# Kernel optimization log

Hardware: AMD Instinct MI355X
Metric: run time of the kernel (lower is better)

Reference implementation:

```python
import jax, jax.numpy as jnp
import numpy as np

N_EMBD = 512
HEAD_SIZE = 64
B, T = 256, 256


def setup_inputs() -> dict:
    key = jax.random.key(0)
    ks = jax.random.split(key, 7)
    s = 1.0 / np.sqrt(N_EMBD)
    return {
        "x": jax.random.normal(ks[0], (B, T, N_EMBD), dtype=jnp.float32),
        "Wk": jax.random.uniform(ks[1], (N_EMBD, HEAD_SIZE), jnp.float32, -s, s),
        "bk": jax.random.uniform(ks[2], (HEAD_SIZE,), jnp.float32, -s, s),
        "Wq": jax.random.uniform(ks[3], (N_EMBD, HEAD_SIZE), jnp.float32, -s, s),
        "bq": jax.random.uniform(ks[4], (HEAD_SIZE,), jnp.float32, -s, s),
        "Wv": jax.random.uniform(ks[5], (N_EMBD, HEAD_SIZE), jnp.float32, -s, s),
        "bv": jax.random.uniform(ks[6], (HEAD_SIZE,), jnp.float32, -s, s),
    }


def reference(x, Wk, bk, Wq, bq, Wv, bv):
    # Single-head causal self-attention (dropout = identity in eval mode).
    Bq, Tq, C = x.shape
    k = x @ Wk + bk        # [B, T, H]
    q = x @ Wq + bq        # [B, T, H]
    v = x @ Wv + bv        # [B, T, H]
    scale = 1.0 / jnp.sqrt(jnp.asarray(k.shape[-1], x.dtype))
    scores = jnp.einsum('bth,bsh->bts', q, k) * scale  # [B, T, T]
    causal = jnp.tril(jnp.ones((Tq, Tq), dtype=bool))
    scores = jnp.where(causal, scores, -jnp.inf)
    attn = jax.nn.softmax(scores, axis=-1)
    return jnp.einsum('bts,bsh->bth', attn, v)  # [B, T, H]
```

## Files before the change

kernel.cpp:

```cpp
#include <hip/hip_runtime.h>
#include <stdint.h>

typedef __attribute__((ext_vector_type(8))) short bf16x8;
typedef __attribute__((ext_vector_type(4))) float f32x4;

#if __has_builtin(__builtin_amdgcn_exp2f)
#define EXP2F(x) __builtin_amdgcn_exp2f(x)
#else
#define EXP2F(x) exp2f(x)
#endif

__device__ __forceinline__ short f2bf(float f) {
    union { float f; uint32_t u; } c; c.f = f;
    return (short)((c.u + 0x7fffu + ((c.u >> 16) & 1u)) >> 16);
}

typedef __attribute__((address_space(1))) void gvoid;
typedef __attribute__((address_space(3))) void lvoid;
__device__ __forceinline__ void async_cp16(const void* g, void* l) {
    __builtin_amdgcn_global_load_lds((gvoid*)g, (lvoid*)l, 16, 0, 0);
}

__global__ void prep_kernel(const float* __restrict__ Wk, const float* __restrict__ bk,
                            const float* __restrict__ Wq, const float* __restrict__ bq,
                            const float* __restrict__ Wv, const float* __restrict__ bv,
                            short* __restrict__ Wt2g, float* __restrict__ bcat) {
    const int col = blockIdx.x;
    const float* W; const float* bb; int c0;
    if (col < 64)       { W = Wk; bb = bk; c0 = col; }
    else if (col < 128) { W = Wq; bb = bq; c0 = col - 64; }
    else                { W = Wv; bb = bv; c0 = col - 128; }
    for (int c = threadIdx.x; c < 512; c += blockDim.x)
        Wt2g[(c >> 5) * (192 * 32) + col * 32 + (c & 31)] = f2bf(W[(size_t)c * 64 + c0]);
    if (threadIdx.x == 0) bcat[col] = bb[c0];
}

#define PSTR 40

__global__ __launch_bounds__(1024, 4) void fused_kernel(
    const float* __restrict__ x, const short* __restrict__ Wt2g,
    const float* __restrict__ bcat, float* __restrict__ out) {
    extern __shared__ __align__(16) char smem[];

    const int tid = threadIdx.x;
    const int wave = tid >> 6, lane = tid & 63;
    const int quad = lane >> 4, l16 = lane & 15;
    const int b = blockIdx.x;

    const int rg = wave >> 2, cg = wave & 3;

    f32x4 acc[4][3];
#pragma unroll
    for (int m = 0; m < 4; m++)
#pragma unroll
        for (int j = 0; j < 3; j++) acc[m][j] = (f32x4){0.f, 0.f, 0.f, 0.f};

    const float* xg = x + ((size_t)b * 256 + wave * 16 + l16) * 512 + quad * 8;

#define STAGE_W(kc, bufp)                                                           \
    if (wave < 12) {                                                                \
        async_cp16(Wt2g + (size_t)(kc) * 6144 + wave * 512 + lane * 8,              \
                   smem + 32768 + (bufp) * 12288 + wave * 1024);                    \
    }

    STAGE_W(0, 0)
    f32x4 xr0 = *(const f32x4*)xg;
    f32x4 xr1 = *(const f32x4*)(xg + 4);
    {
        bf16x8 v;
#pragma unroll
        for (int i = 0; i < 4; i++) { v[i] = f2bf(xr0[i]); v[4 + i] = f2bf(xr1[i]); }
        *(bf16x8*)((short*)smem + wave * 512 + lane * 8) = v;
    }
    __syncthreads();

    for (int kc = 0; kc < 16; kc++) {
        const int buf = kc & 1;
        if (kc < 15) {
            STAGE_W(kc + 1, buf ^ 1)
            xr0 = *(const f32x4*)(xg + (kc + 1) * 32);
            xr1 = *(const f32x4*)(xg + (kc + 1) * 32 + 4);
        }
        const short* wb = (const short*)(smem + 32768 + buf * 12288);
        bf16x8 bfr0 = *(const bf16x8*)&wb[(cg * 48 + l16) * 32 + quad * 8];
        bf16x8 bfr1 = *(const bf16x8*)&wb[(cg * 48 + 16 + l16) * 32 + quad * 8];
        bf16x8 bfr2 = *(const bf16x8*)&wb[(cg * 48 + 32 + l16) * 32 + quad * 8];
        const short* xbr = (const short*)smem + buf * 8192;
#pragma unroll
        for (int m = 0; m < 4; m++) {
            bf16x8 afr = *(const bf16x8*)&xbr[(rg * 4 + m) * 512 + lane * 8];
            acc[m][0] = __builtin_amdgcn_mfma_f32_16x16x32_bf16(afr, bfr0, acc[m][0], 0, 0, 0);
            acc[m][1] = __builtin_amdgcn_mfma_f32_16x16x32_bf16(afr, bfr1, acc[m][1], 0, 0, 0);
            acc[m][2] = __builtin_amdgcn_mfma_f32_16x16x32_bf16(afr, bfr2, acc[m][2], 0, 0, 0);
        }
        if (kc < 15) {
            bf16x8 v;
#pragma unroll
            for (int i = 0; i < 4; i++) { v[i] = f2bf(xr0[i]); v[4 + i] = f2bf(xr1[i]); }
            *(bf16x8*)((short*)smem + (buf ^ 1) * 8192 + wave * 512 + lane * 8) = v;
        }
        __syncthreads();
    }

    short* Ks  = (short*)smem;
    short* Qs  = (short*)(smem + 32768);
    short* Vts = (short*)(smem + 65536);
    short* Ps  = (short*)(smem + 98304);
#pragma unroll
    for (int j = 0; j < 3; j++) {
        const int col = cg * 48 + j * 16 + l16;
        const float bias = bcat[col];
        const int h = col & 63;
        const int sel = col >> 6;
#pragma unroll
        for (int m = 0; m < 4; m++) {
#pragma unroll
            for (int r = 0; r < 4; r++) {
                const short v = f2bf(acc[m][j][r] + bias);
                const int row = rg * 64 + m * 16 + quad * 4 + r;
                if (sel == 0)
                    Ks[row * 64 + (((h >> 3) ^ (row & 7)) << 3) + (h & 7)] = v;
                else if (sel == 1)
                    Qs[row * 64 + (((h >> 3) ^ (row & 7)) << 3) + (h & 7)] = v;
                else
                    Vts[h * 256 + (((row >> 3) ^ (h & 7)) << 3) + (row & 7)] = v;
            }
        }
    }
    __syncthreads();

    const int qt = ((wave >> 2) << 2) | ((wave & 3) ^ (wave >> 2));
    const float sc2 = 0.125f * 1.44269504088896340736f;
    short* myP = Ps + wave * (16 * PSTR);

    const int qrow = qt * 16 + l16;
    const int sw = l16 & 7;
    bf16x8 qf0 = *(const bf16x8*)&Qs[qrow * 64 + ((quad ^ sw) << 3)];
    bf16x8 qf1 = *(const bf16x8*)&Qs[qrow * 64 + (((4 + quad) ^ sw) << 3)];

    f32x4 St[16];
#pragma unroll
    for (int i = 0; i < 16; i++) St[i] = (f32x4){0.f, 0.f, 0.f, 0.f};
#pragma unroll
    for (int nt = 0; nt < 16; nt++) if (nt <= qt) {
        const int krow = nt * 16 + l16;
        bf16x8 kf0 = *(const bf16x8*)&Ks[krow * 64 + ((quad ^ sw) << 3)];
        bf16x8 kf1 = *(const bf16x8*)&Ks[krow * 64 + (((4 + quad) ^ sw) << 3)];
        St[nt] = __builtin_amdgcn_mfma_f32_16x16x32_bf16(qf0, kf0, St[nt], 0, 0, 0);
        St[nt] = __builtin_amdgcn_mfma_f32_16x16x32_bf16(qf1, kf1, St[nt], 0, 0, 0);
    }

    const int rowq = qt * 16 + quad * 4;
    float mx[4], ls[4];
#pragma unroll
    for (int r = 0; r < 4; r++) mx[r] = -3.0e38f;
#pragma unroll
    for (int nt = 0; nt < 16; nt++) if (nt <= qt) {
        const int cs = nt * 16 + l16;
#pragma unroll
        for (int r = 0; r < 4; r++) {
            float s = (cs <= rowq + r) ? St[nt][r] * sc2 : -3.0e38f;
            St[nt][r] = s;
            mx[r] = fmaxf(mx[r], s);
        }
    }
#pragma unroll
    for (int d = 1; d < 16; d <<= 1)
#pragma unroll
        for (int r = 0; r < 4; r++)
            mx[r] = fmaxf(mx[r], __shfl_xor(mx[r], d, 64));
#pragma unroll
    for (int r = 0; r < 4; r++) ls[r] = 0.f;
#pragma unroll
    for (int nt = 0; nt < 16; nt++) if (nt <= qt) {
#pragma unroll
        for (int r = 0; r < 4; r++) {
            float p = EXP2F(St[nt][r] - mx[r]);
            St[nt][r] = p;
            ls[r] += p;
        }
    }
#pragma unroll
    for (int d = 1; d < 16; d <<= 1)
#pragma unroll
        for (int r = 0; r < 4; r++)
            ls[r] += __shfl_xor(ls[r], d, 64);

    f32x4 O[4];
#pragma unroll
    for (int i = 0; i < 4; i++) O[i] = (f32x4){0.f, 0.f, 0.f, 0.f};
    const int nch = (qt + 2) >> 1;
#pragma unroll
    for (int c2 = 0; c2 < 8; c2++) if (c2 < nch) {
#pragma unroll
        for (int t2i = 0; t2i < 2; t2i++) {
            const int nt = c2 * 2 + t2i;
#pragma unroll
            for (int r = 0; r < 4; r++)
                myP[(quad * 4 + r) * PSTR + t2i * 16 + l16] = f2bf(St[nt][r]);
        }
        bf16x8 pf = *(const bf16x8*)&myP[l16 * PSTR + quad * 8];
#pragma unroll
        for (int ht = 0; ht < 4; ht++) {
            const int h = ht * 16 + l16;
            bf16x8 vf = *(const bf16x8*)&Vts[h * 256 + (((c2 * 4 + quad) ^ (h & 7)) << 3)];
            O[ht] = __builtin_amdgcn_mfma_f32_16x16x32_bf16(pf, vf, O[ht], 0, 0, 0);
        }
    }

    float rls[4];
#pragma unroll
    for (int r = 0; r < 4; r++) rls[r] = 1.0f / ls[r];
#pragma unroll
    for (int ht = 0; ht < 4; ht++)
#pragma unroll
        for (int r = 0; r < 4; r++)
            out[((size_t)b * 256 + rowq + r) * 64 + ht * 16 + l16] = O[ht][r] * rls[r];
#undef STAGE_W
}

extern "C" void kernel_launch(void* const* d_in, const int* in_sizes, int n_in,
                              void* d_out, int out_size, void* d_ws, size_t ws_size,
                              hipStream_t stream) {
    const float* x  = (const float*)d_in[0];
    const float* Wk = (const float*)d_in[1];
    const float* bk = (const float*)d_in[2];
    const float* Wq = (const float*)d_in[3];
    const float* bq = (const float*)d_in[4];
    const float* Wv = (const float*)d_in[5];
    const float* bv = (const float*)d_in[6];
    float* out = (float*)d_out;

    char* ws = (char*)d_ws;
    short* Wt2g = (short*)(ws);
    float* bcat = (float*)(ws + 196608);

    const int smem_bytes = 118784;
    (void)hipFuncSetAttribute((const void*)fused_kernel,
                              hipFuncAttributeMaxDynamicSharedMemorySize, smem_bytes);

    prep_kernel<<<192, 256, 0, stream>>>(Wk, bk, Wq, bq, Wv, bv, Wt2g, bcat);
    fused_kernel<<<256, 1024, smem_bytes, stream>>>(x, Wt2g, bcat, out);
}
```

Baseline: 222.0 us.

## Stream x as fp32 via async LDS copies in a triple-buffered projection pipeline

The QKV projection loop now loads x as raw fp32 straight into LDS with global_load_lds, and the W tiles come the same way. It uses three stages with explicit vmcnt waits and raw barriers in place of the register-staged double buffer. Conversion to bf16 moves to the LDS-read side, and both the x and W tiles use XOR swizzles to avoid bank conflicts. The aim is to keep more loads in flight and take the global load latency off the critical path. The cost is more LDS (135 KB), which limits residency to one block per CU, plus hand-tuned wait counts that are fragile.

```diff
diff --git a/kernel.cpp b/kernel.cpp
--- a/kernel.cpp
+++ b/kernel.cpp
@@ -30,8 +30,11 @@
     if (col < 64)       { W = Wk; bb = bk; c0 = col; }
     else if (col < 128) { W = Wq; bb = bq; c0 = col - 64; }
     else                { W = Wv; bb = bv; c0 = col - 128; }
-    for (int c = threadIdx.x; c < 512; c += blockDim.x)
-        Wt2g[(c >> 5) * (192 * 32) + col * 32 + (c & 31)] = f2bf(W[(size_t)c * 64 + c0]);
+    for (int c = threadIdx.x; c < 512; c += blockDim.x) {
+        const int k5 = c & 31;
+        Wt2g[(c >> 5) * 6144 + col * 32 + ((((k5 >> 3) ^ (col & 3)) << 3)) + (k5 & 7)] =
+            f2bf(W[(size_t)c * 64 + c0]);
+    }
     if (threadIdx.x == 0) bcat[col] = bb[c0];
 }
 
@@ -46,7 +49,6 @@
     const int wave = tid >> 6, lane = tid & 63;
     const int quad = lane >> 4, l16 = lane & 15;
     const int b = blockIdx.x;
-
     const int rg = wave >> 2, cg = wave & 3;
 
     f32x4 acc[4][3];
@@ -55,52 +57,70 @@
 #pragma unroll
         for (int j = 0; j < 3; j++) acc[m][j] = (f32x4){0.f, 0.f, 0.f, 0.f};
 
-    const float* xg = x + ((size_t)b * 256 + wave * 16 + l16) * 512 + quad * 8;
-
-#define STAGE_W(kc, bufp)                                                           \
-    if (wave < 12) {                                                                \
-        async_cp16(Wt2g + (size_t)(kc) * 6144 + wave * 512 + lane * 8,              \
-                   smem + 32768 + (bufp) * 12288 + wave * 1024);                    \
-    }
-
-    STAGE_W(0, 0)
-    f32x4 xr0 = *(const f32x4*)xg;
-    f32x4 xr1 = *(const f32x4*)(xg + 4);
-    {
-        bf16x8 v;
-#pragma unroll
-        for (int i = 0; i < 4; i++) { v[i] = f2bf(xr0[i]); v[4 + i] = f2bf(xr1[i]); }
-        *(bf16x8*)((short*)smem + wave * 512 + lane * 8) = v;
-    }
+    const float* xsrc = x + (size_t)b * 256 * 512;
+    const int xr = lane >> 3, xsl = lane & 7;
+    const int bsw = (quad ^ (l16 & 3)) << 3;
+    const int xq0 = ((2 * quad) ^ (l16 & 7)) << 2;
+    const int xq1 = ((2 * quad + 1) ^ (l16 & 7)) << 2;
+
+#define XS(d) (smem + (d) * 32768)
+#define WSB(d) (smem + 98304 + (d) * 12288)
+#define STAGE(kc, d)                                                                     \
+    {                                                                                    \
+        async_cp16(xsrc + (size_t)(wave * 8 + xr) * 512 + (kc) * 32 + ((xsl ^ xr) << 2), \
+                   XS(d) + wave * 1024);                                                 \
+        async_cp16(xsrc + (size_t)((wave + 16) * 8 + xr) * 512 + (kc) * 32 +             \
+                       ((xsl ^ xr) << 2),                                                \
+                   XS(d) + (wave + 16) * 1024);                                          \
+        if (wave < 12)                                                                   \
+            async_cp16(Wt2g + (size_t)(kc) * 6144 + wave * 512 + lane * 8,               \
+                       WSB(d) + wave * 1024);                                            \
+    }
+#define FENCE() asm volatile("" ::: "memory")
+
+    auto COMPUTE = [&](int d) {
+        const short* wb = (const short*)WSB(d);
+        bf16x8 bf0 = *(const bf16x8*)&wb[(cg * 48 + l16) * 32 + bsw];
+        bf16x8 bf1 = *(const bf16x8*)&wb[(cg * 48 + 16 + l16) * 32 + bsw];
+        bf16x8 bf2 = *(const bf16x8*)&wb[(cg * 48 + 32 + l16) * 32 + bsw];
+        const float* xb = (const float*)XS(d);
+        const int rbase = (rg * 64 + l16) * 32;
+#pragma unroll
+        for (int m = 0; m < 4; m++) {
+            f32x4 u0 = *(const f32x4*)&xb[rbase + m * 512 + xq0];
+            f32x4 u1 = *(const f32x4*)&xb[rbase + m * 512 + xq1];
+            bf16x8 a;
+#pragma unroll
+            for (int i = 0; i < 4; i++) { a[i] = f2bf(u0[i]); a[4 + i] = f2bf(u1[i]); }
+            acc[m][0] = __builtin_amdgcn_mfma_f32_16x16x32_bf16(a, bf0, acc[m][0], 0, 0, 0);
+            acc[m][1] = __builtin_amdgcn_mfma_f32_16x16x32_bf16(a, bf1, acc[m][1], 0, 0, 0);
+            acc[m][2] = __builtin_amdgcn_mfma_f32_16x16x32_bf16(a, bf2, acc[m][2], 0, 0, 0);
+        }
+    };
+
+    STAGE(0, 0) STAGE(1, 1) STAGE(2, 2)
+
+    for (int kc = 0; kc < 14; ++kc) {
+        const int d = kc % 3;
+        if (wave < 12) asm volatile("s_waitcnt vmcnt(6)" ::: "memory");
+        else           asm volatile("s_waitcnt vmcnt(4)" ::: "memory");
+        __builtin_amdgcn_s_barrier();
+        FENCE();
+        COMPUTE(d);
+        __builtin_amdgcn_s_barrier();
+        FENCE();
+        if (kc < 13) STAGE(kc + 3, d)
+    }
+    if (wave < 12) asm volatile("s_waitcnt vmcnt(3)" ::: "memory");
+    else           asm volatile("s_waitcnt vmcnt(2)" ::: "memory");
+    __builtin_amdgcn_s_barrier();
+    FENCE();
+    COMPUTE(2);
+    asm volatile("s_waitcnt vmcnt(0)" ::: "memory");
+    __builtin_amdgcn_s_barrier();
+    FENCE();
+    COMPUTE(0);
     __syncthreads();
-
-    for (int kc = 0; kc < 16; kc++) {
-        const int buf = kc & 1;
-        if (kc < 15) {
-            STAGE_W(kc + 1, buf ^ 1)
-            xr0 = *(const f32x4*)(xg + (kc + 1) * 32);
-            xr1 = *(const f32x4*)(xg + (kc + 1) * 32 + 4);
-        }
-        const short* wb = (const short*)(smem + 32768 + buf * 12288);
-        bf16x8 bfr0 = *(const bf16x8*)&wb[(cg * 48 + l16) * 32 + quad * 8];
-        bf16x8 bfr1 = *(const bf16x8*)&wb[(cg * 48 + 16 + l16) * 32 + quad * 8];
-        bf16x8 bfr2 = *(const bf16x8*)&wb[(cg * 48 + 32 + l16) * 32 + quad * 8];
-        const short* xbr = (const short*)smem + buf * 8192;
-#pragma unroll
-        for (int m = 0; m < 4; m++) {
-            bf16x8 afr = *(const bf16x8*)&xbr[(rg * 4 + m) * 512 + lane * 8];
-            acc[m][0] = __builtin_amdgcn_mfma_f32_16x16x32_bf16(afr, bfr0, acc[m][0], 0, 0, 0);
-            acc[m][1] = __builtin_amdgcn_mfma_f32_16x16x32_bf16(afr, bfr1, acc[m][1], 0, 0, 0);
-            acc[m][2] = __builtin_amdgcn_mfma_f32_16x16x32_bf16(afr, bfr2, acc[m][2], 0, 0, 0);
-        }
-        if (kc < 15) {
-            bf16x8 v;
-#pragma unroll
-            for (int i = 0; i < 4; i++) { v[i] = f2bf(xr0[i]); v[4 + i] = f2bf(xr1[i]); }
-            *(bf16x8*)((short*)smem + (buf ^ 1) * 8192 + wave * 512 + lane * 8) = v;
-        }
-        __syncthreads();
-    }
 
     short* Ks  = (short*)smem;
     short* Qs  = (short*)(smem + 32768);
@@ -216,7 +236,10 @@
 #pragma unroll
         for (int r = 0; r < 4; r++)
             out[((size_t)b * 256 + rowq + r) * 64 + ht * 16 + l16] = O[ht][r] * rls[r];
-#undef STAGE_W
+#undef STAGE
+#undef XS
+#undef WSB
+#undef FENCE
 }
 
 extern "C" void kernel_launch(void* const* d_in, const int* in_sizes, int n_in,
@@ -235,7 +258,7 @@
     short* Wt2g = (short*)(ws);
     float* bcat = (float*)(ws + 196608);
 
-    const int smem_bytes = 118784;
+    const int smem_bytes = 135168;
     (void)hipFuncSetAttribute((const void*)fused_kernel,
                               hipFuncAttributeMaxDynamicSharedMemorySize, smem_bytes);
 
```

New measurement: 222.3 us. About the same (+0.1%).
